# Kernel optimization log

Hardware: AMD Instinct MI355X
Metric: run time of the kernel (lower is better)

## Reference

```python
import jax, jax.numpy as jnp
import numpy as np

B, S, D, H = 2, 1024, 1024, 16
HD = D // H
WINDOW = 256
FFN = 4 * D


def setup_inputs() -> dict:
    key = jax.random.key(0)
    ks = jax.random.split(key, 12)
    xav = lambda k, o, i: jax.random.normal(k, (o, i), jnp.float32) * np.sqrt(2.0 / (o + i))
    return {
        "x": jax.random.normal(ks[0], (B, S, D), jnp.float32),
        "wq": xav(ks[1], D, D), "bq": jnp.zeros((D,), jnp.float32),
        "wk": xav(ks[2], D, D), "bk": jnp.zeros((D,), jnp.float32),
        "wv": xav(ks[3], D, D), "bv": jnp.zeros((D,), jnp.float32),
        "wo": xav(ks[4], D, D), "bo": jnp.zeros((D,), jnp.float32),
        "attn_norm_w": jnp.ones((D,), jnp.float32),
        "ffn_norm_w": jnp.ones((D,), jnp.float32),
        "gate_w": xav(ks[5], FFN, D),
        "up_w": xav(ks[6], FFN, D),
        "down_w": xav(ks[7], D, FFN),
    }


def _rms(x, w):
    return x * jax.lax.rsqrt(jnp.mean(x * x, axis=-1, keepdims=True) + 1e-6) * w


def _rotate_half(x):
    x1, x2 = jnp.split(x, 2, axis=-1)
    return jnp.concatenate([-x2, x1], axis=-1)


def _rope_cos_sin(seq_len, head_dim):
    inv_freq = 1.0 / (10000.0 ** (jnp.arange(0, head_dim, 2, dtype=jnp.float32) / head_dim))
    freqs = jnp.arange(seq_len, dtype=jnp.float32)[:, None] * inv_freq[None, :]  # [S, HD/2]
    emb = jnp.concatenate([freqs, freqs], axis=-1)  # [S, HD]
    return jnp.cos(emb)[None, None], jnp.sin(emb)[None, None]  # [1,1,S,HD]


def reference(x, wq, bq, wk, bk, wv, bv, wo, bo, attn_norm_w, ffn_norm_w, gate_w, up_w, down_w):
    b, s, d = x.shape
    scale = 1.0 / np.sqrt(HD)
    residual = x
    h = _rms(x, attn_norm_w)
    q = (h @ wq.T + bq).reshape(b, s, H, HD).transpose(0, 2, 1, 3)  # [B,H,S,HD]
    k = (h @ wk.T + bk).reshape(b, s, H, HD).transpose(0, 2, 1, 3)
    v = (h @ wv.T + bv).reshape(b, s, H, HD).transpose(0, 2, 1, 3)
    cos, sin = _rope_cos_sin(s, HD)
    q = q * cos + _rotate_half(q) * sin
    k = k * cos + _rotate_half(k) * sin
    scores = jnp.einsum("bhqd,bhkd->bhqk", q, k) * scale  # dense [B,H,S,S]
    i = jnp.arange(s)[:, None]
    j = jnp.arange(s)[None, :]
    local_mask = (j <= i) & (i - j < WINDOW)  # causal sliding window
    scores = jnp.where(local_mask[None, None], scores, -jnp.inf)
    attn = jax.nn.softmax(scores, axis=-1)
    out = jnp.einsum("bhqk,bhkd->bhqd", attn, v)
    out = out.transpose(0, 2, 1, 3).reshape(b, s, d) @ wo.T + bo
    x = residual + out
    residual = x
    h = _rms(x, ffn_norm_w)
    ffn = (jax.nn.silu(h @ gate_w.T) * (h @ up_w.T)) @ down_w.T
    return (residual + ffn, attn)
```

## Files before the change

kernel.cpp:

```cpp
#include <hip/hip_runtime.h>

typedef unsigned short u16;
typedef unsigned int u32;
typedef __attribute__((ext_vector_type(8))) short short8;
typedef __attribute__((ext_vector_type(4))) float f32x4;

__device__ __forceinline__ float b2fu(u32 u) {
  union { u32 i; float f; } v; v.i = u << 16; return v.f;
}
__device__ __forceinline__ u16 f2bu(float f) {
  union { float f; u32 i; } v; v.f = f;
  u32 r = (v.i + 0x7fffu + ((v.i >> 16) & 1u)) >> 16;
  return (u16)r;
}
__device__ __forceinline__ void gl_lds16(const void* g, void* l) {
  __builtin_amdgcn_global_load_lds((const __attribute__((address_space(1))) void*)g,
                                   (__attribute__((address_space(3))) void*)l, 16, 0, 0);
}
__device__ __forceinline__ short8 ld_lds_b8(const u16* p) {
  uint2 a = *(const uint2*)p;
  uint2 b = *(const uint2*)(p + 4);
  union { u32 u[4]; short8 s; } v;
  v.u[0] = a.x; v.u[1] = a.y; v.u[2] = b.x; v.u[3] = b.y;
  return v.s;
}

__global__ __launch_bounds__(256) void cvt_weights(
    const float* __restrict__ wq, const float* __restrict__ wk,
    const float* __restrict__ wv, const float* __restrict__ wo,
    const float* __restrict__ wg, const float* __restrict__ wu,
    const float* __restrict__ wd, u16* __restrict__ dst,
    const float* __restrict__ bq, const float* __restrict__ bk,
    const float* __restrict__ bv, float* __restrict__ bqkv)
{
  if (blockIdx.x >= 16384) {
    const int s = blockIdx.x - 16384;
    const float* bsrc = (s == 0) ? bq : (s == 1) ? bk : bv;
    const int o = threadIdx.x * 4;
    *(float4*)(bqkv + s * 1024 + o) = *(const float4*)(bsrc + o);
    return;
  }
  size_t e = ((size_t)blockIdx.x * 256 + threadIdx.x) * 4;
  size_t seg = e >> 20;
  const float* src; size_t soff;
  if      (seg == 0) { src = wq; soff = e; }
  else if (seg == 1) { src = wk; soff = e - ((size_t)1 << 20); }
  else if (seg == 2) { src = wv; soff = e - ((size_t)2 << 20); }
  else if (seg == 3) { src = wo; soff = e - ((size_t)3 << 20); }
  else if (seg < 12) {
    size_t idx = e - ((size_t)4 << 20);
    int rc = (int)(idx >> 10);
    int col = (int)(idx & 1023);
    int bi = rc >> 5, j = rc & 31;
    if (j < 16) { src = wg; soff = (size_t)(bi * 16 + j) * 1024 + col; }
    else        { src = wu; soff = (size_t)(bi * 16 + j - 16) * 1024 + col; }
  }
  else { src = wd; soff = e - ((size_t)12 << 20); }
  float4 v = *(const float4*)(src + soff);
  *(ushort4*)(dst + e) = make_ushort4(f2bu(v.x), f2bu(v.y), f2bu(v.z), f2bu(v.w));
}

__global__ __launch_bounds__(256) void rmsnorm_kernel(
    const float* __restrict__ x, const float* __restrict__ w, u16* __restrict__ out)
{
  const int row = blockIdx.x;
  const int t = threadIdx.x;
  float4 v = ((const float4*)(x + (size_t)row * 1024))[t];
  float ss = v.x * v.x + v.y * v.y + v.z * v.z + v.w * v.w;
#pragma unroll
  for (int m = 32; m > 0; m >>= 1) ss += __shfl_xor(ss, m, 64);
  __shared__ float red[4];
  if ((t & 63) == 0) red[t >> 6] = ss;
  __syncthreads();
  float tot = red[0] + red[1] + red[2] + red[3];
  float r = rsqrtf(tot * (1.0f / 1024.0f) + 1e-6f);
  float4 wv = ((const float4*)w)[t];
  ushort4 o = make_ushort4(f2bu(v.x * r * wv.x), f2bu(v.y * r * wv.y),
                           f2bu(v.z * r * wv.z), f2bu(v.w * r * wv.w));
  ((ushort4*)(out + (size_t)row * 1024))[t] = o;
}

template<int TMB, int TNB, int EPI, bool HAS_BIAS, bool HAS_RES, bool SPLIT>
__global__ __launch_bounds__(256) void gemm_bt(
    const u16* __restrict__ A, const u16* __restrict__ B, float* __restrict__ C,
    const float* __restrict__ bias, const float* __restrict__ res,
    int M, int N, int K, int lda,
    u16* __restrict__ P0, u16* __restrict__ P1, u16* __restrict__ P2)
{
  constexpr int BK = 32;
  constexpr int WTM = TMB / 2, WTN = TNB / 2;
  constexpr int MT = WTM / 16, NT = WTN / 16;
  __shared__ u16 As[TMB * BK];
  __shared__ u16 Bs[TNB * BK];
  const int t = threadIdx.x;
  const int w = t >> 6, l = t & 63;
  const int wm = (w >> 1) * WTM, wn = (w & 1) * WTN;
  const int lr = l & 15, lq = l >> 4;
  const int tile_m = blockIdx.y * TMB, tile_n = blockIdx.x * TNB;
  const int kb = SPLIT ? blockIdx.z * K : 0;
  if (SPLIT) C += (size_t)blockIdx.z * M * N;

  f32x4 acc[MT][NT] = {};

  const int sr = t >> 2;
  const int sc8 = (t & 3) * 8;
  const u16* Ab = A + (size_t)(tile_m + sr) * lda + kb + sc8;
  const u16* Bb = B + (size_t)(tile_n + sr) * lda + kb + sc8;

  for (int kk = 0; kk < K; kk += BK) {
#pragma unroll
    for (int i = 0; i < TMB / 64; ++i)
      gl_lds16(Ab + kk + (size_t)i * 64 * lda, &As[t * 8 + i * 2048]);
#pragma unroll
    for (int i = 0; i < TNB / 64; ++i)
      gl_lds16(Bb + kk + (size_t)i * 64 * lda, &Bs[t * 8 + i * 2048]);
    __syncthreads();
    short8 af[MT], bfr[NT];
#pragma unroll
    for (int mt = 0; mt < MT; ++mt)
      af[mt] = *(const short8*)&As[(wm + mt * 16 + lr) * BK + lq * 8];
#pragma unroll
    for (int nt = 0; nt < NT; ++nt)
      bfr[nt] = *(const short8*)&Bs[(wn + nt * 16 + lr) * BK + lq * 8];
#pragma unroll
    for (int mt = 0; mt < MT; ++mt)
#pragma unroll
      for (int nt = 0; nt < NT; ++nt)
        acc[mt][nt] = __builtin_amdgcn_mfma_f32_16x16x32_bf16(af[mt], bfr[nt], acc[mt][nt], 0, 0, 0);
    __syncthreads();
  }

  if (EPI == 0) {
#pragma unroll
    for (int nt = 0; nt < NT; ++nt) {
      const int col = tile_n + wn + nt * 16 + lr;
      const float bv = HAS_BIAS ? bias[col] : 0.0f;
#pragma unroll
      for (int mt = 0; mt < MT; ++mt) {
        const int row0 = tile_m + wm + mt * 16 + lq * 4;
#pragma unroll
        for (int r = 0; r < 4; ++r) {
          const size_t off = (size_t)(row0 + r) * N + col;
          float v = acc[mt][nt][r] + bv;
          if (HAS_RES) v += res[off];
          C[off] = v;
        }
      }
    }
  } else if (EPI == 1) {
    const int colbase = tile_n + wn;
    const int seg = colbase >> 10;
    const int h = (colbase >> 6) & 15;
    u16* dstb = (seg == 0) ? P0 : (seg == 1) ? P1 : P2;
    float bv[NT];
#pragma unroll
    for (int nt = 0; nt < NT; ++nt) bv[nt] = bias[colbase + nt * 16 + lr];
#pragma unroll
    for (int mt = 0; mt < MT; ++mt) {
      const int row0 = tile_m + wm + mt * 16 + lq * 4;
#pragma unroll
      for (int r = 0; r < 4; ++r) {
        const int row = row0 + r;
        const int s = row & 1023, b = row >> 10;
        u16* dst = dstb + (((size_t)(b * 16 + h) << 10) + s) * 64;
        if (seg < 2) {
#pragma unroll
          for (int np = 0; np < 2; ++np) {
            const int i = np * 16 + lr;
            const float th = (float)s * exp2f(-0.4152410118609203f * (float)i);
            float sn, cs; __sincosf(th, &sn, &cs);
            const float g0 = acc[mt][np][r] + bv[np];
            const float g2 = acc[mt][np + 2][r] + bv[np + 2];
            dst[i]      = f2bu(g0 * cs - g2 * sn);
            dst[i + 32] = f2bu(g2 * cs + g0 * sn);
          }
        } else {
#pragma unroll
          for (int nt = 0; nt < NT; ++nt)
            dst[nt * 16 + lr] = f2bu(acc[mt][nt][r] + bv[nt]);
        }
      }
    }
  } else {
#pragma unroll
    for (int nt = 0; nt < NT; nt += 2) {
      const int feat = (((tile_n + wn + nt * 16) >> 5) << 4) + lr;
#pragma unroll
      for (int mt = 0; mt < MT; ++mt) {
        const int row0 = tile_m + wm + mt * 16 + lq * 4;
#pragma unroll
        for (int r = 0; r < 4; ++r) {
          const float g = acc[mt][nt][r];
          const float u = acc[mt][nt + 1][r];
          const float a = g / (1.0f + __expf(-g)) * u;
          P0[(size_t)(row0 + r) * (N >> 1) + feat] = f2bu(a);
        }
      }
    }
  }
}

__global__ __launch_bounds__(256) void reduce4_kernel(
    const float* __restrict__ p, const float* __restrict__ res, float* __restrict__ out)
{
  const size_t i = ((size_t)blockIdx.x * 256 + threadIdx.x) * 4;
  float4 a = *(const float4*)(p + i);
  float4 b = *(const float4*)(p + i + 2097152);
  float4 c = *(const float4*)(p + i + 2 * 2097152);
  float4 d = *(const float4*)(p + i + 3 * 2097152);
  float4 r = *(const float4*)(res + i);
  float4 o;
  o.x = r.x + a.x + b.x + c.x + d.x;
  o.y = r.y + a.y + b.y + c.y + d.y;
  o.z = r.z + a.z + b.z + c.z + d.z;
  o.w = r.w + a.w + b.w + c.w + d.w;
  *(float4*)(out + i) = o;
}

#define KP 68
#define PP 292

__global__ __launch_bounds__(256) void attn_kernel(
    const u16* __restrict__ qb, const u16* __restrict__ kb, const u16* __restrict__ vb,
    float* __restrict__ probs, u16* __restrict__ ctx)
{
  __shared__ u16 Kbuf[288 * KP];
  __shared__ u16 Vbuf[288 * KP];
  __shared__ float smax[2][32];
  __shared__ float ssum[2][32];
  u16* Pbuf = Kbuf;

  const int blk = blockIdx.x;
  const int qt = blk & 31, bh = blk >> 5;
  const int b = bh >> 4, h = bh & 15;
  const int q0 = qt << 5;
  const int kstart = (q0 > 255) ? (q0 - 255) : 0;
  const int span = q0 + 32 - kstart;
  const int t = threadIdx.x;
  const int w = t >> 6, l = t & 63;
  const int lr = l & 15, lq = l >> 4;
  const int mw = w & 1, nh = w >> 1;
  const size_t bhS = (size_t)bh << 10;

  {
    const u16* kg = kb + ((bhS + (size_t)kstart) << 6);
    const u16* vg = vb + ((bhS + (size_t)kstart) << 6);
    for (int idx = t; idx < 288 * 8; idx += 256) {
      const int r = idx >> 3, c = (idx & 7) << 3;
      uint4 kv4 = make_uint4(0, 0, 0, 0), vv4 = make_uint4(0, 0, 0, 0);
      if (r < span) {
        kv4 = *(const uint4*)&kg[(r << 6) + c];
        vv4 = *(const uint4*)&vg[(r << 6) + c];
      }
      *(uint2*)&Kbuf[r * KP + c]     = make_uint2(kv4.x, kv4.y);
      *(uint2*)&Kbuf[r * KP + c + 4] = make_uint2(kv4.z, kv4.w);
      *(uint2*)&Vbuf[r * KP + c]     = make_uint2(vv4.x, vv4.y);
      *(uint2*)&Vbuf[r * KP + c + 4] = make_uint2(vv4.z, vv4.w);
    }
  }
  short8 qa0, qa1;
  {
    const u16* qrow = qb + ((bhS + (size_t)(q0 + mw * 16 + lr)) << 6) + lq * 8;
    qa0 = *(const short8*)qrow;
    qa1 = *(const short8*)(qrow + 32);
  }
  __syncthreads();

  f32x4 acc[9];
#pragma unroll
  for (int i = 0; i < 9; ++i) acc[i] = (f32x4){0.f, 0.f, 0.f, 0.f};
#pragma unroll
  for (int i = 0; i < 9; ++i) {
    const int nt = nh + 2 * i;
    const u16* kr = &Kbuf[(nt * 16 + lr) * KP + lq * 8];
    short8 kf0 = ld_lds_b8(kr);
    short8 kf1 = ld_lds_b8(kr + 32);
    acc[i] = __builtin_amdgcn_mfma_f32_16x16x32_bf16(qa0, kf0, acc[i], 0, 0, 0);
    acc[i] = __builtin_amdgcn_mfma_f32_16x16x32_bf16(qa1, kf1, acc[i], 0, 0, 0);
  }

  const int rbase = mw * 16 + lq * 4;
  float rmax[4] = {-1e30f, -1e30f, -1e30f, -1e30f};
#pragma unroll
  for (int i = 0; i < 9; ++i) {
    const int jg = kstart + (nh + 2 * i) * 16 + lr;
#pragma unroll
    for (int r = 0; r < 4; ++r) {
      const int q = q0 + rbase + r;
      const bool valid = (jg >= q - 255) && (jg <= q);
      const float v = valid ? acc[i][r] * 0.125f : -1e30f;
      acc[i][r] = v;
      rmax[r] = fmaxf(rmax[r], v);
    }
  }
#pragma unroll
  for (int r = 0; r < 4; ++r) {
    float m_ = rmax[r];
    m_ = fmaxf(m_, __shfl_xor(m_, 1, 64));
    m_ = fmaxf(m_, __shfl_xor(m_, 2, 64));
    m_ = fmaxf(m_, __shfl_xor(m_, 4, 64));
    m_ = fmaxf(m_, __shfl_xor(m_, 8, 64));
    rmax[r] = m_;
  }
  if (lr == 0) {
#pragma unroll
    for (int r = 0; r < 4; ++r) smax[nh][rbase + r] = rmax[r];
  }
  __syncthreads();
#pragma unroll
  for (int r = 0; r < 4; ++r)
    rmax[r] = fmaxf(smax[0][rbase + r], smax[1][rbase + r]);
  float rsum[4] = {0.f, 0.f, 0.f, 0.f};
#pragma unroll
  for (int i = 0; i < 9; ++i)
#pragma unroll
    for (int r = 0; r < 4; ++r) {
      const float p = exp2f((acc[i][r] - rmax[r]) * 1.44269504f);
      acc[i][r] = p;
      rsum[r] += p;
    }
#pragma unroll
  for (int r = 0; r < 4; ++r) {
    float s_ = rsum[r];
    s_ += __shfl_xor(s_, 1, 64);
    s_ += __shfl_xor(s_, 2, 64);
    s_ += __shfl_xor(s_, 4, 64);
    s_ += __shfl_xor(s_, 8, 64);
    rsum[r] = s_;
  }
  if (lr == 0) {
#pragma unroll
    for (int r = 0; r < 4; ++r) ssum[nh][rbase + r] = rsum[r];
  }
  __syncthreads();

  float inv4[4];
#pragma unroll
  for (int r = 0; r < 4; ++r)
    inv4[r] = 1.0f / (ssum[0][rbase + r] + ssum[1][rbase + r]);
#pragma unroll
  for (int i = 0; i < 9; ++i) {
    const int nt = nh + 2 * i;
#pragma unroll
    for (int r = 0; r < 4; ++r)
      Pbuf[(rbase + r) * PP + nt * 16 + lr] = f2bu(acc[i][r] * inv4[r]);
  }
  __syncthreads();

  {
    const int row = t >> 3;
    const int q = q0 + row;
    const int c0 = (t & 7) << 7;
    const int lo = q - 255;
    float* prow = probs + ((bhS + (size_t)q) << 10) + c0;
    const u16* pr = &Pbuf[row * PP];
#pragma unroll 4
    for (int cc = 0; cc < 128; cc += 4) {
      const int c = c0 + cc;
      float4 o;
      o.x = (c + 0 >= lo && c + 0 <= q) ? b2fu(pr[c + 0 - kstart]) : 0.0f;
      o.y = (c + 1 >= lo && c + 1 <= q) ? b2fu(pr[c + 1 - kstart]) : 0.0f;
      o.z = (c + 2 >= lo && c + 2 <= q) ? b2fu(pr[c + 2 - kstart]) : 0.0f;
      o.w = (c + 3 >= lo && c + 3 <= q) ? b2fu(pr[c + 3 - kstart]) : 0.0f;
      *(float4*)&prow[cc] = o;
    }
  }

  const int n0 = (w >> 1) * 2;
  f32x4 oacc[2] = {};
#pragma unroll
  for (int ks = 0; ks < 9; ++ks) {
    short8 pa = ld_lds_b8(&Pbuf[(mw * 16 + lr) * PP + ks * 32 + lq * 8]);
#pragma unroll
    for (int nn = 0; nn < 2; ++nn) {
      const int d = (n0 + nn) * 16 + lr;
      union { u16 u[8]; short8 s; } bf_;
#pragma unroll
      for (int jj = 0; jj < 8; ++jj)
        bf_.u[jj] = Vbuf[(ks * 32 + lq * 8 + jj) * KP + d];
      oacc[nn] = __builtin_amdgcn_mfma_f32_16x16x32_bf16(pa, bf_.s, oacc[nn], 0, 0, 0);
    }
  }
#pragma unroll
  for (int nn = 0; nn < 2; ++nn) {
    const int d = (n0 + nn) * 16 + lr;
#pragma unroll
    for (int r = 0; r < 4; ++r) {
      const int q = q0 + rbase + r;
      ctx[(((size_t)(b * 1024 + q)) << 10) + (h << 6) + d] = f2bu(oacc[nn][r]);
    }
  }
}

extern "C" void kernel_launch(void* const* d_in, const int* in_sizes, int n_in,
                              void* d_out, int out_size, void* d_ws, size_t ws_size,
                              hipStream_t stream) {
  (void)in_sizes; (void)n_in; (void)out_size; (void)ws_size;
  const float* x   = (const float*)d_in[0];
  const float* wq  = (const float*)d_in[1];
  const float* bq  = (const float*)d_in[2];
  const float* wk  = (const float*)d_in[3];
  const float* bk  = (const float*)d_in[4];
  const float* wv  = (const float*)d_in[5];
  const float* bv  = (const float*)d_in[6];
  const float* wo  = (const float*)d_in[7];
  const float* bo  = (const float*)d_in[8];
  const float* anw = (const float*)d_in[9];
  const float* fnw = (const float*)d_in[10];
  const float* wg  = (const float*)d_in[11];
  const float* wu  = (const float*)d_in[12];
  const float* wd  = (const float*)d_in[13];

  char* ws = (char*)d_ws;
  u16*   wbf  = (u16*)ws;
  float* bqkv = (float*)(ws + ((size_t)32 << 20));
  u16*   h1   = (u16*)(ws + ((size_t)32 << 20) + (16 << 10));
  char*  R    = ws + ((size_t)36 << 20) + (16 << 10);
  u16*   qbp  = (u16*)R;
  u16*   kbp  = (u16*)(R + ((size_t)4 << 20));
  u16*   vbp  = (u16*)(R + ((size_t)8 << 20));
  u16*   ctx  = (u16*)(R + ((size_t)12 << 20));
  float* x1   = (float*)(R + ((size_t)16 << 20));
  u16*   h2   = (u16*)(R + ((size_t)24 << 20));
  u16*   act  = (u16*)(R + ((size_t)28 << 20));
  float* pbuf = (float*)(R + ((size_t)44 << 20));

  float* out0  = (float*)d_out;
  float* probs = (float*)d_out + 2097152;

  cvt_weights<<<16387, 256, 0, stream>>>(wq, wk, wv, wo, wg, wu, wd, wbf,
                                          bq, bk, bv, bqkv);

  rmsnorm_kernel<<<2048, 256, 0, stream>>>(x, anw, h1);
  gemm_bt<64, 128, 1, true, false, false><<<dim3(24, 32), 256, 0, stream>>>(
      h1, wbf, nullptr, bqkv, nullptr, 2048, 3072, 1024, 1024, qbp, kbp, vbp);
  attn_kernel<<<1024, 256, 0, stream>>>(qbp, kbp, vbp, probs, ctx);
  gemm_bt<64, 128, 0, true, true, false><<<dim3(8, 32), 256, 0, stream>>>(
      ctx, wbf + ((size_t)3 << 20), x1, bo, x, 2048, 1024, 1024, 1024,
      nullptr, nullptr, nullptr);

  rmsnorm_kernel<<<2048, 256, 0, stream>>>(x1, fnw, h2);
  gemm_bt<128, 128, 2, false, false, false><<<dim3(64, 16), 256, 0, stream>>>(
      h2, wbf + ((size_t)4 << 20), nullptr, nullptr, nullptr, 2048, 8192, 1024, 1024,
      act, nullptr, nullptr);
  gemm_bt<64, 128, 0, false, false, true><<<dim3(8, 32, 4), 256, 0, stream>>>(
      act, wbf + ((size_t)12 << 20), pbuf, nullptr, nullptr, 2048, 1024, 1024, 4096,
      nullptr, nullptr, nullptr);
  reduce4_kernel<<<2048, 256, 0, stream>>>(pbuf, x1, out0);
}
```

Measured before the change: 423.1 us.

## Fuse attn RMSNorm into weight conversion, split-K output projection, enlarge QKV tile

The first RMSNorm is folded into the weight-conversion launch as extra blocks, which removes one kernel launch. The QKV GEMM moves to 128x128 tiles. The output projection now uses split-K of 2 into a partial buffer, followed by a new reduce2 kernel that adds bias and residual. Together these aim to cut launch overhead and raise occupancy for the small output GEMM. The cost is an extra round trip of partial sums through memory and a larger workspace.

```diff
diff --git a/kernel.cpp b/kernel.cpp
--- a/kernel.cpp
+++ b/kernel.cpp
@@ -25,14 +25,34 @@
   return v.s;
 }
 
-__global__ __launch_bounds__(256) void cvt_weights(
+__global__ __launch_bounds__(256) void cvt_front(
     const float* __restrict__ wq, const float* __restrict__ wk,
     const float* __restrict__ wv, const float* __restrict__ wo,
     const float* __restrict__ wg, const float* __restrict__ wu,
     const float* __restrict__ wd, u16* __restrict__ dst,
     const float* __restrict__ bq, const float* __restrict__ bk,
-    const float* __restrict__ bv, float* __restrict__ bqkv)
-{
+    const float* __restrict__ bv, float* __restrict__ bqkv,
+    const float* __restrict__ x, const float* __restrict__ anw,
+    u16* __restrict__ h1)
+{
+  __shared__ float red[4];
+  if (blockIdx.x >= 16387) {
+    const int row = blockIdx.x - 16387;
+    const int t = threadIdx.x;
+    float4 v = ((const float4*)(x + (size_t)row * 1024))[t];
+    float ss = v.x * v.x + v.y * v.y + v.z * v.z + v.w * v.w;
+#pragma unroll
+    for (int m = 32; m > 0; m >>= 1) ss += __shfl_xor(ss, m, 64);
+    if ((t & 63) == 0) red[t >> 6] = ss;
+    __syncthreads();
+    float tot = red[0] + red[1] + red[2] + red[3];
+    float r = rsqrtf(tot * (1.0f / 1024.0f) + 1e-6f);
+    float4 wv4 = ((const float4*)anw)[t];
+    ushort4 o = make_ushort4(f2bu(v.x * r * wv4.x), f2bu(v.y * r * wv4.y),
+                             f2bu(v.z * r * wv4.z), f2bu(v.w * r * wv4.w));
+    ((ushort4*)(h1 + (size_t)row * 1024))[t] = o;
+    return;
+  }
   if (blockIdx.x >= 16384) {
     const int s = blockIdx.x - 16384;
     const float* bsrc = (s == 0) ? bq : (s == 1) ? bk : bv;
@@ -198,6 +218,23 @@
       }
     }
   }
+}
+
+__global__ __launch_bounds__(256) void reduce2_kernel(
+    const float* __restrict__ p, const float* __restrict__ bias,
+    const float* __restrict__ res, float* __restrict__ out)
+{
+  const size_t i = ((size_t)blockIdx.x * 256 + threadIdx.x) * 4;
+  float4 a = *(const float4*)(p + i);
+  float4 b = *(const float4*)(p + i + 2097152);
+  float4 r = *(const float4*)(res + i);
+  float4 bv = *(const float4*)(bias + (i & 1023));
+  float4 o;
+  o.x = r.x + bv.x + a.x + b.x;
+  o.y = r.y + bv.y + a.y + b.y;
+  o.z = r.z + bv.z + a.z + b.z;
+  o.w = r.w + bv.w + a.w + b.w;
+  *(float4*)(out + i) = o;
 }
 
 __global__ __launch_bounds__(256) void reduce4_kernel(
@@ -424,20 +461,21 @@
   u16*   h2   = (u16*)(R + ((size_t)24 << 20));
   u16*   act  = (u16*)(R + ((size_t)28 << 20));
   float* pbuf = (float*)(R + ((size_t)44 << 20));
+  float* pbuf2= (float*)(R + ((size_t)76 << 20));
 
   float* out0  = (float*)d_out;
   float* probs = (float*)d_out + 2097152;
 
-  cvt_weights<<<16387, 256, 0, stream>>>(wq, wk, wv, wo, wg, wu, wd, wbf,
-                                          bq, bk, bv, bqkv);
-
-  rmsnorm_kernel<<<2048, 256, 0, stream>>>(x, anw, h1);
-  gemm_bt<64, 128, 1, true, false, false><<<dim3(24, 32), 256, 0, stream>>>(
+  cvt_front<<<18435, 256, 0, stream>>>(wq, wk, wv, wo, wg, wu, wd, wbf,
+                                       bq, bk, bv, bqkv, x, anw, h1);
+
+  gemm_bt<128, 128, 1, true, false, false><<<dim3(24, 16), 256, 0, stream>>>(
       h1, wbf, nullptr, bqkv, nullptr, 2048, 3072, 1024, 1024, qbp, kbp, vbp);
   attn_kernel<<<1024, 256, 0, stream>>>(qbp, kbp, vbp, probs, ctx);
-  gemm_bt<64, 128, 0, true, true, false><<<dim3(8, 32), 256, 0, stream>>>(
-      ctx, wbf + ((size_t)3 << 20), x1, bo, x, 2048, 1024, 1024, 1024,
+  gemm_bt<64, 128, 0, false, false, true><<<dim3(8, 32, 2), 256, 0, stream>>>(
+      ctx, wbf + ((size_t)3 << 20), pbuf2, nullptr, nullptr, 2048, 1024, 512, 1024,
       nullptr, nullptr, nullptr);
+  reduce2_kernel<<<2048, 256, 0, stream>>>(pbuf2, bo, x, x1);
 
   rmsnorm_kernel<<<2048, 256, 0, stream>>>(x1, fnw, h2);
   gemm_bt<128, 128, 2, false, false, false><<<dim3(64, 16), 256, 0, stream>>>(
```

After: 432.3 us. 2.2% more time.
